# Kernel tuning notes

Hardware: AMD Instinct MI355X
Metric: run time of the kernel (lower is better)

The kernel has to match this reference:

```python
import jax, jax.numpy as jnp
import numpy as np

B, N, E_PER = 512, 256, 8192          # graphs, nodes per graph, edges per graph
FIN, H, K, FOUT = 128, 32, 16, 10     # in_channels, hidden, num clusters, out_channels
EPS = 1e-15


def setup_inputs() -> dict:
    key = jax.random.key(0)
    ks = jax.random.split(key, 12)
    x = jax.random.normal(ks[0], (B * N, FIN), jnp.float32)
    # intra-graph random edges, then offset into the global node index space
    src = jax.random.randint(ks[1], (B, E_PER), 0, N)
    dst = jax.random.randint(ks[2], (B, E_PER), 0, N)
    offs = (jnp.arange(B) * N)[:, None]
    edge_index = jnp.stack([(src + offs).reshape(-1), (dst + offs).reshape(-1)]).astype(jnp.int64)
    batch = jnp.repeat(jnp.arange(B), N).astype(jnp.int64)

    def lin(k, fin, fout):
        return (jax.random.normal(k, (fin, fout), jnp.float32) / np.sqrt(fin)).astype(jnp.float32)

    params = {
        'W_lin1': lin(ks[3], FIN, H), 'b_lin1': jnp.zeros((H,), jnp.float32),
        'W_rel1': lin(ks[4], H, H), 'b_rel1': jnp.zeros((H,), jnp.float32),
        'W_root1': lin(ks[5], H, H),
        'W_pool': lin(ks[6], H, K), 'b_pool': jnp.zeros((K,), jnp.float32),
        'W_rel2': lin(ks[7], H, H), 'b_rel2': jnp.zeros((H,), jnp.float32),
        'W_root2': lin(ks[8], H, H),
        'W_lin2': lin(ks[9], H, H), 'b_lin2': jnp.zeros((H,), jnp.float32),
        'W_lin3': lin(ks[10], H, FOUT), 'b_lin3': jnp.zeros((FOUT,), jnp.float32),
    }
    return {'x': x, 'edge_index': edge_index, 'batch': batch, **params}


def _densify(x, edge_index, batch):
    """to_dense_adj + to_dense_batch: [total,F] -> [B,N,F], [B,N,N], [B,N]."""
    n_total = x.shape[0]
    counts = jax.ops.segment_sum(jnp.ones((n_total,), jnp.int32), batch, num_segments=B)
    offsets = jnp.concatenate([jnp.zeros((1,), jnp.int32), jnp.cumsum(counts)[:-1]])
    pos = jnp.arange(n_total) - offsets[batch]            # position of node inside its graph
    eb = batch[edge_index[0]]                             # graph id of each edge
    adj = jnp.zeros((B, N, N), jnp.float32).at[eb, pos[edge_index[0]], pos[edge_index[1]]].add(1.0)
    xd = jnp.zeros((B, N, x.shape[1]), jnp.float32).at[batch, pos].set(x)
    mask = jnp.zeros((B, N), jnp.float32).at[batch, pos].set(1.0)
    return xd, adj, mask


def _dense_graph_conv(x, adj, W_rel, b_rel, W_root):
    # PyG DenseGraphConv(aggr='add'): lin_rel(adj @ x) + lin_root(x)
    return jnp.einsum('bnm,bmh,hk->bnk', adj, x, W_rel) + b_rel + x @ W_root


def _dense_mincut_pool(x, adj, s, mask):
    s = jax.nn.softmax(s, axis=-1)
    x = x * mask[..., None]
    s = s * mask[..., None]
    out = jnp.einsum('bnk,bnh->bkh', s, x)                        # s^T x
    out_adj = jnp.einsum('bnk,bnm,bmj->bkj', s, adj, s)           # s^T A s
    mincut_num = jnp.einsum('bkk->b', out_adj)
    d_flat = adj.sum(-1)                                          # degree
    mincut_den = jnp.einsum('bnk,bn,bnk->b', s, d_flat, s)        # trace(s^T D s)
    mincut_loss = jnp.mean(-(mincut_num / mincut_den))
    ss = jnp.einsum('bnk,bnj->bkj', s, s)
    ss_norm = jnp.linalg.norm(ss, axis=(-1, -2), keepdims=True)
    i_s = jnp.eye(K, dtype=jnp.float32)
    ortho_loss = jnp.mean(jnp.linalg.norm(ss / ss_norm - i_s / jnp.sqrt(jnp.float32(K)), axis=(-1, -2)))
    # zero diagonal, symmetric degree normalization
    diag_mask = 1.0 - i_s
    out_adj = out_adj * diag_mask
    d = jnp.sqrt(out_adj.sum(-1))[:, None, :] + EPS               # [B,1,K]
    out_adj = out_adj / d / jnp.swapaxes(d, 1, 2)
    return out, out_adj, mincut_loss, ortho_loss


def reference(x, edge_index, batch, W_lin1, b_lin1, W_rel1, b_rel1, W_root1,
              W_pool, b_pool, W_rel2, b_rel2, W_root2, W_lin2, b_lin2, W_lin3, b_lin3):
    xd, adj, mask = _densify(x, edge_index, batch)
    h = xd @ W_lin1 + b_lin1                                      # lin1
    h = _dense_graph_conv(h, adj, W_rel1, b_rel1, W_root1)        # conv1
    s2 = h @ W_pool + b_pool                                      # pool2
    h, adj_p, mincut_loss2, ortho_loss2 = _dense_mincut_pool(h, adj, s2, mask)
    h = _dense_graph_conv(h, adj_p, W_rel2, b_rel2, W_root2)      # conv2
    h = h.sum(axis=1)                                             # readout sum over clusters
    h = jax.nn.relu(h @ W_lin2 + b_lin2)
    h = h @ W_lin3 + b_lin3
    return jax.nn.log_softmax(h, axis=-1), mincut_loss2, ortho_loss2
```

## Files before the change

kernel.cpp:

```cpp
#include <hip/hip_runtime.h>

#define NB 512
#define NN 256
#define EPG 8192
#define FINC 128

typedef float f32x4 __attribute__((ext_vector_type(4)));
typedef short s16x8 __attribute__((ext_vector_type(8)));

__device__ __forceinline__ float bf2f(unsigned short u) {
  union { unsigned int i; float f; } x; x.i = ((unsigned int)u) << 16; return x.f;
}
__device__ __forceinline__ unsigned short f2bf(float f) {
  union { float f; unsigned int i; } x; x.f = f;
  unsigned int r = x.i + 0x7fffu + ((x.i >> 16) & 1u);
  return (unsigned short)(r >> 16);
}
__device__ __forceinline__ short ftrunc_bf(float f) {
  union { float f; unsigned int i; } x; x.f = f;
  return (short)(x.i >> 16);
}

struct Params {
  const void* x; const void* ei;
  const void *wl1, *bl1, *wr1, *br1, *wro1, *wp, *bp;
  const void *wr2, *br2, *wro2, *wl2, *bl2, *wl3, *bl3;
  float* out; float* ws;
};

__device__ __forceinline__ bool detect_bf16(const void* p) {
  const unsigned short* pw = (const unsigned short*)p;
  int sane = 0;
  for (int i = 0; i < 64; ++i) {
    unsigned e = (pw[i] >> 7) & 0xFFu;
    sane += (e > 96u && e < 132u) ? 1 : 0;
  }
  return sane >= 56;
}
__device__ __forceinline__ bool detect_i64(const void* p) {
  const int* pi = (const int*)p + EPG;
  int ok = 0;
  for (int i = 0; i < 32; ++i) ok += (pi[i] >= 256 && pi[i] < 512) ? 1 : 0;
  return ok < 24;
}
__device__ __forceinline__ float ldf(const void* p, int i, bool bf) {
  return bf ? bf2f(((const unsigned short*)p)[i]) : ((const float*)p)[i];
}

#define SMEM_TOTAL 81920

__global__ __launch_bounds__(1024, 8) void mincut_main(Params P) {
  extern __shared__ char smem[];
  const int t = threadIdx.x;
  const int b = blockIdx.x;

  const bool BF  = detect_bf16(P.wr1);
  const bool I64 = detect_i64(P.ei);

  float* pbuf   = (float*)(smem + 0);
  float* oadjb  = (float*)(smem + 2048);
  float* ssb    = (float*)(smem + 3072);
  float* qbuf   = (float*)(smem + 4096);
  float* ddb    = (float*)(smem + 6144);
  float* h2b    = (float*)(smem + 6208);
  float* rb     = (float*)(smem + 8256);
  float* yb     = (float*)(smem + 8384);
  float* lgb    = (float*)(smem + 8512);
  float* scr    = (float*)(smem + 8704);
  float* rel2f  = (float*)(smem + 9216);
  float* root2f = (float*)(smem + 13312);
  float* lin2f  = (float*)(smem + 17408);
  float* lin3f  = (float*)(smem + 21504);
  float* brel2f = (float*)(smem + 22784);
  float* blin2f = (float*)(smem + 22912);
  float* blin3f = (float*)(smem + 23040);
  float* pbufH  = (float*)(smem + 24576);
  float* pbufL  = (float*)(smem + 26624);
  float* oadjH  = (float*)(smem + 28672);
  float* oadjL  = (float*)(smem + 29696);
  float* ssA    = (float*)(smem + 30720);
  float* ssX    = (float*)(smem + 31744);
  unsigned short* h0T  = (unsigned short*)(smem + 33792);
  unsigned short* yTl  = (unsigned short*)(smem + 33792);
  unsigned short* h1Th = (unsigned short*)(smem + 33792);
  unsigned short* w1t  = (unsigned short*)(smem + 50688);
  unsigned short* zT   = (unsigned short*)(smem + 50688);
  unsigned short* sTh  = (unsigned short*)(smem + 50688);
  unsigned short* sTl  = (unsigned short*)(smem + 59136);
  unsigned short* wrelTh = (unsigned short*)(smem + 67584);
  unsigned short* wrelTl = (unsigned short*)(smem + 70144);
  unsigned short* wrootT = (unsigned short*)(smem + 72704);
  float* blin1f = (float*)(smem + 75264);
  unsigned short* yTh = (unsigned short*)(smem + 67584);
  unsigned short* taT = (unsigned short*)(smem + 67584);
  unsigned short* wpoolTh = (unsigned short*)(smem + 76032);
  unsigned short* wpoolTl = (unsigned short*)(smem + 77184);
  unsigned short* m1Th    = (unsigned short*)(smem + 78336);
  unsigned short* m1Tl    = (unsigned short*)(smem + 79488);
  float*          scrE    = (float*)(smem + 79488);
  unsigned short* m2Th    = (unsigned short*)(smem + 80640);
  float*          bMf     = (float*)(smem + 81792);
  unsigned short* brel1h  = (unsigned short*)(smem + 81856);

  const int wv = t >> 6, lane = t & 63;
  const int lm = lane & 15, quad = lane >> 4;
  const int mbase = wv * 16;

  {
    uint4 z = {0u, 0u, 0u, 0u};
    for (int i = t; i < 2112; i += 1024) ((uint4*)smem)[i] = z;
  }
  for (int e = t; e < 4096; e += 1024) {
    int k = e >> 5, c = e & 31;
    w1t[c * 136 + k] = f2bf(ldf(P.wl1, e, BF));
  }
  {
    int k = t >> 5, c = t & 31;
    float wr = ldf(P.wr1, t, BF);
    unsigned short hi = f2bf(wr);
    wrelTh[c * 40 + k] = hi;
    wrelTl[c * 40 + k] = f2bf(wr - bf2f(hi));
    wrootT[c * 40 + k] = f2bf(ldf(P.wro1, t, BF));
  }
  if (t < 512) {
    int m = t >> 4, c = t & 15;
    float w = ldf(P.wp, t, BF);
    unsigned short hi = f2bf(w);
    wpoolTh[c * 36 + m] = hi;
    wpoolTl[c * 36 + m] = f2bf(w - bf2f(hi));
  }
  if (t < 32) { blin1f[t] = ldf(P.bl1, t, BF); brel1h[t] = f2bf(ldf(P.br1, t, BF)); }
  __syncthreads();

  if (I64) {
    const uint4* s4 = (const uint4*)((const long long*)P.ei + (size_t)b * EPG) + t * 4;
    const uint4* d4 = (const uint4*)((const long long*)P.ei + (size_t)NB * EPG + (size_t)b * EPG) + t * 4;
    #pragma unroll
    for (int i = 0; i < 4; ++i) {
      uint4 a = s4[i], c = d4[i];
      unsigned n0 = (a.x & 255u) * 264u + (c.x & 255u);
      unsigned n1 = (a.z & 255u) * 264u + (c.z & 255u);
      atomicAdd((unsigned int*)(smem + ((n0 >> 3) << 2)), 1u << ((n0 & 7u) * 4u));
      atomicAdd((unsigned int*)(smem + ((n1 >> 3) << 2)), 1u << ((n1 & 7u) * 4u));
    }
  } else {
    const uint4* s4 = (const uint4*)((const int*)P.ei + (size_t)b * EPG) + t * 2;
    const uint4* d4 = (const uint4*)((const int*)P.ei + (size_t)NB * EPG + (size_t)b * EPG) + t * 2;
    #pragma unroll
    for (int i = 0; i < 2; ++i) {
      uint4 a = s4[i], c = d4[i];
      unsigned n0 = (a.x & 255u) * 264u + (c.x & 255u);
      unsigned n1 = (a.y & 255u) * 264u + (c.y & 255u);
      unsigned n2 = (a.z & 255u) * 264u + (c.z & 255u);
      unsigned n3 = (a.w & 255u) * 264u + (c.w & 255u);
      atomicAdd((unsigned int*)(smem + ((n0 >> 3) << 2)), 1u << ((n0 & 7u) * 4u));
      atomicAdd((unsigned int*)(smem + ((n1 >> 3) << 2)), 1u << ((n1 & 7u) * 4u));
      atomicAdd((unsigned int*)(smem + ((n2 >> 3) << 2)), 1u << ((n2 & 7u) * 4u));
      atomicAdd((unsigned int*)(smem + ((n3 >> 3) << 2)), 1u << ((n3 & 7u) * 4u));
    }
  }

  {
    f32x4 acc[2] = {{0.f,0.f,0.f,0.f},{0.f,0.f,0.f,0.f}};
    const size_t node = (size_t)(b * 256 + mbase + lm);
    #pragma unroll
    for (int ks = 0; ks < 4; ++ks) {
      const int k0 = ks * 32 + quad * 8;
      s16x8 a;
      if (BF) {
        a = *(const s16x8*)((const unsigned short*)P.x + node * 128 + k0);
      } else {
        const float* xp = (const float*)P.x + node * 128 + k0;
        f32x4 v0 = *(const f32x4*)xp;
        f32x4 v1 = *(const f32x4*)(xp + 4);
        #pragma unroll
        for (int j = 0; j < 4; ++j) { a[j] = (short)f2bf(v0[j]); a[4 + j] = (short)f2bf(v1[j]); }
      }
      #pragma unroll
      for (int ct = 0; ct < 2; ++ct) {
        s16x8 bh = *(const s16x8*)(w1t + (ct * 16 + lm) * 136 + k0);
        acc[ct] = __builtin_amdgcn_mfma_f32_16x16x32_bf16(a, bh, acc[ct], 0, 0, 0);
      }
    }
    #pragma unroll
    for (int ct = 0; ct < 2; ++ct) {
      const int c = ct * 16 + lm;
      float bias = blin1f[c];
      #pragma unroll
      for (int r = 0; r < 4; ++r)
        h0T[c * 264 + mbase + quad * 4 + r] = f2bf(acc[ct][r] + bias);
    }
  }

  if (wv == 2 || wv == 3) {
    const int mb = (wv - 2) * 16;
    s16x8 Ah, Al;
    #pragma unroll
    for (int j = 0; j < 8; ++j) {
      int k = quad * 8 + j;
      Ah[j] = (short)wrelTh[k * 40 + mb + lm];
      Al[j] = (short)wrelTl[k * 40 + mb + lm];
    }
    s16x8 Bh, Bl;
    ((uint2*)&Bh)[0] = *(const uint2*)(wpoolTh + lm * 36 + quad * 8);
    ((uint2*)&Bh)[1] = *(const uint2*)(wpoolTh + lm * 36 + quad * 8 + 4);
    ((uint2*)&Bl)[0] = *(const uint2*)(wpoolTl + lm * 36 + quad * 8);
    ((uint2*)&Bl)[1] = *(const uint2*)(wpoolTl + lm * 36 + quad * 8 + 4);
    f32x4 acc = {0.f, 0.f, 0.f, 0.f};
    acc = __builtin_amdgcn_mfma_f32_16x16x32_bf16(Ah, Bh, acc, 0, 0, 0);
    acc = __builtin_amdgcn_mfma_f32_16x16x32_bf16(Al, Bh, acc, 0, 0, 0);
    acc = __builtin_amdgcn_mfma_f32_16x16x32_bf16(Ah, Bl, acc, 0, 0, 0);
    #pragma unroll
    for (int r = 0; r < 4; ++r) {
      int m = mb + quad * 4 + r;
      unsigned short hi = f2bf(acc[r]);
      m1Th[lm * 36 + m] = hi;
      m1Tl[lm * 36 + m] = f2bf(acc[r] - bf2f(hi));
    }
  }
  if (wv == 4 || wv == 5) {
    const int mb = (wv - 4) * 16;
    s16x8 Ah;
    #pragma unroll
    for (int j = 0; j < 8; ++j) Ah[j] = (short)wrootT[(quad * 8 + j) * 40 + mb + lm];
    s16x8 Bh, Bl;
    ((uint2*)&Bh)[0] = *(const uint2*)(wpoolTh + lm * 36 + quad * 8);
    ((uint2*)&Bh)[1] = *(const uint2*)(wpoolTh + lm * 36 + quad * 8 + 4);
    ((uint2*)&Bl)[0] = *(const uint2*)(wpoolTl + lm * 36 + quad * 8);
    ((uint2*)&Bl)[1] = *(const uint2*)(wpoolTl + lm * 36 + quad * 8 + 4);
    f32x4 acc = {0.f, 0.f, 0.f, 0.f};
    acc = __builtin_amdgcn_mfma_f32_16x16x32_bf16(Ah, Bh, acc, 0, 0, 0);
    acc = __builtin_amdgcn_mfma_f32_16x16x32_bf16(Ah, Bl, acc, 0, 0, 0);
    #pragma unroll
    for (int r = 0; r < 4; ++r) m2Th[lm * 36 + (mb + quad * 4 + r)] = f2bf(acc[r]);
  }
  if (wv == 6 && lane < 16) {
    float acc = ldf(P.bp, lane, BF);
    #pragma unroll 8
    for (int m = 0; m < 32; ++m)
      acc += bf2f(brel1h[m]) * (bf2f(wpoolTh[lane * 36 + m]) + bf2f(wpoolTl[lane * 36 + m]));
    bMf[lane] = acc;
  }
  __syncthreads();

  f32x4 racc[2] = {{0.f,0.f,0.f,0.f},{0.f,0.f,0.f,0.f}};
  f32x4 yacc = {0.f,0.f,0.f,0.f}, macc = {0.f,0.f,0.f,0.f};
  {
    s16x8 Ah;
    #pragma unroll
    for (int j = 0; j < 8; ++j) Ah[j] = (short)h0T[(quad * 8 + j) * 264 + mbase + lm];
    f32x4 zacc[2] = {{0.f,0.f,0.f,0.f},{0.f,0.f,0.f,0.f}};
    #pragma unroll
    for (int ct = 0; ct < 2; ++ct) {
      const int c = ct * 16 + lm;
      s16x8 brh = *(const s16x8*)(wrelTh + c * 40 + quad * 8);
      s16x8 brl = *(const s16x8*)(wrelTl + c * 40 + quad * 8);
      s16x8 bro = *(const s16x8*)(wrootT + c * 40 + quad * 8);
      zacc[ct] = __builtin_amdgcn_mfma_f32_16x16x32_bf16(Ah, brh, zacc[ct], 0, 0, 0);
      zacc[ct] = __builtin_amdgcn_mfma_f32_16x16x32_bf16(Ah, brl, zacc[ct], 0, 0, 0);
      racc[ct] = __builtin_amdgcn_mfma_f32_16x16x32_bf16(Ah, bro, racc[ct], 0, 0, 0);
    }
    s16x8 Bm1h, Bm1l, Bm2;
    ((uint2*)&Bm1h)[0] = *(const uint2*)(m1Th + lm * 36 + quad * 8);
    ((uint2*)&Bm1h)[1] = *(const uint2*)(m1Th + lm * 36 + quad * 8 + 4);
    ((uint2*)&Bm1l)[0] = *(const uint2*)(m1Tl + lm * 36 + quad * 8);
    ((uint2*)&Bm1l)[1] = *(const uint2*)(m1Tl + lm * 36 + quad * 8 + 4);
    ((uint2*)&Bm2)[0]  = *(const uint2*)(m2Th + lm * 36 + quad * 8);
    ((uint2*)&Bm2)[1]  = *(const uint2*)(m2Th + lm * 36 + quad * 8 + 4);
    yacc = __builtin_amdgcn_mfma_f32_16x16x32_bf16(Ah, Bm1h, yacc, 0, 0, 0);
    yacc = __builtin_amdgcn_mfma_f32_16x16x32_bf16(Ah, Bm1l, yacc, 0, 0, 0);
    macc = __builtin_amdgcn_mfma_f32_16x16x32_bf16(Ah, Bm2, macc, 0, 0, 0);
    #pragma unroll
    for (int ct = 0; ct < 2; ++ct)
      #pragma unroll
      for (int r = 0; r < 4; ++r)
        zT[(ct * 16 + lm) * 264 + mbase + quad * 4 + r] = f2bf(zacc[ct][r]);
  }
  __syncthreads();

  #pragma unroll
  for (int r = 0; r < 4; ++r) {
    int node = mbase + quad * 4 + r;
    unsigned short hi = f2bf(yacc[r]);
    yTh[lm * 264 + node] = hi;
    yTl[lm * 264 + node] = f2bf(yacc[r] - bf2f(hi));
  }
  __syncthreads();

  f32x4 h1v[2], sval;
  {
    f32x4 h1acc[2] = { racc[0], racc[1] };
    f32x4 lacc = macc;
    unsigned dsum = 0;
    const char* arow = smem + (mbase + lm) * 132;
    #pragma unroll
    for (int ks = 0; ks < 8; ++ks) {
      unsigned d = *(const unsigned int*)(arow + ks * 16 + quad * 4);
      unsigned v = (d & 0x0F0F0F0Fu) + ((d >> 4) & 0x0F0F0F0Fu);
      dsum += (v * 0x01010101u) >> 24;
      s16x8 af;
      #pragma unroll
      for (int j = 0; j < 8; ++j) af[j] = ftrunc_bf((float)((d >> (4 * j)) & 15u));
      const int v0 = ks * 32 + quad * 8;
      #pragma unroll
      for (int ct = 0; ct < 2; ++ct) {
        s16x8 bz = *(const s16x8*)(zT + (ct * 16 + lm) * 264 + v0);
        h1acc[ct] = __builtin_amdgcn_mfma_f32_16x16x32_bf16(af, bz, h1acc[ct], 0, 0, 0);
      }
      s16x8 byh = *(const s16x8*)(yTh + lm * 264 + v0);
      s16x8 byl = *(const s16x8*)(yTl + lm * 264 + v0);
      lacc = __builtin_amdgcn_mfma_f32_16x16x32_bf16(af, byh, lacc, 0, 0, 0);
      lacc = __builtin_amdgcn_mfma_f32_16x16x32_bf16(af, byl, lacc, 0, 0, 0);
    }
    dsum += __shfl_xor(dsum, 16, 64);
    dsum += __shfl_xor(dsum, 32, 64);
    float degf = (float)dsum;
    #pragma unroll
    for (int ct = 0; ct < 2; ++ct) {
      float bias = bf2f(brel1h[ct * 16 + lm]);
      #pragma unroll
      for (int r = 0; r < 4; ++r) h1v[ct][r] = h1acc[ct][r] + bias;
    }
    f32x4 lg;
    float bm = bMf[lm];
    #pragma unroll
    for (int r = 0; r < 4; ++r) lg[r] = lacc[r] + bm;
    f32x4 mx = lg;
    #pragma unroll
    for (int m = 1; m <= 8; m <<= 1)
      #pragma unroll
      for (int r = 0; r < 4; ++r) mx[r] = fmaxf(mx[r], __shfl_xor(mx[r], m, 64));
    #pragma unroll
    for (int r = 0; r < 4; ++r) lg[r] = __expf(lg[r] - mx[r]);
    f32x4 sm = lg;
    #pragma unroll
    for (int m = 1; m <= 8; m <<= 1)
      #pragma unroll
      for (int r = 0; r < 4; ++r) sm[r] += __shfl_xor(sm[r], m, 64);
    f32x4 sq;
    #pragma unroll
    for (int r = 0; r < 4; ++r) { sval[r] = lg[r] / sm[r]; sq[r] = sval[r] * sval[r]; }
    #pragma unroll
    for (int m = 1; m <= 8; m <<= 1)
      #pragma unroll
      for (int r = 0; r < 4; ++r) sq[r] += __shfl_xor(sq[r], m, 64);
    {
      int l = lane & 15, src = (l >> 2) << 4;
      float q0 = __shfl(sq[0], src, 64), q1 = __shfl(sq[1], src, 64);
      float q2 = __shfl(sq[2], src, 64), q3 = __shfl(sq[3], src, 64);
      float ssel = (l & 2) ? ((l & 1) ? q3 : q2) : ((l & 1) ? q1 : q0);
      float vden = (lane < 16) ? degf * ssel : 0.f;
      #pragma unroll
      for (int o = 32; o > 0; o >>= 1) vden += __shfl_xor(vden, o, 64);
      if (lane == 0) scrE[wv] = vden;
    }
  }
  __syncthreads();

  #pragma unroll
  for (int ct = 0; ct < 2; ++ct)
    #pragma unroll
    for (int r = 0; r < 4; ++r)
      h1Th[(ct * 16 + lm) * 264 + mbase + quad * 4 + r] = f2bf(h1v[ct][r]);
  #pragma unroll
  for (int r = 0; r < 4; ++r) {
    int node = mbase + quad * 4 + r;
    unsigned short hi = f2bf(sval[r]);
    sTh[lm * 264 + node] = hi;
    sTl[lm * 264 + node] = f2bf(sval[r] - bf2f(hi));
  }
  __syncthreads();

  {
    f32x4 tacc = {0.f, 0.f, 0.f, 0.f};
    const char* arow = smem + (mbase + lm) * 132;
    #pragma unroll
    for (int ks = 0; ks < 8; ++ks) {
      unsigned d = *(const unsigned int*)(arow + ks * 16 + quad * 4);
      s16x8 af;
      #pragma unroll
      for (int j = 0; j < 8; ++j) af[j] = ftrunc_bf((float)((d >> (4 * j)) & 15u));
      const int v0 = ks * 32 + quad * 8;
      s16x8 bh = *(const s16x8*)(sTh + lm * 264 + v0);
      s16x8 bl = *(const s16x8*)(sTl + lm * 264 + v0);
      tacc = __builtin_amdgcn_mfma_f32_16x16x32_bf16(af, bh, tacc, 0, 0, 0);
      tacc = __builtin_amdgcn_mfma_f32_16x16x32_bf16(af, bl, tacc, 0, 0, 0);
    }
    #pragma unroll
    for (int r = 0; r < 4; ++r) taT[lm * 264 + mbase + quad * 4 + r] = f2bf(tacc[r]);
  }
  __syncthreads();

  rel2f[t] = ldf(P.wr2, t, BF);
  root2f[t] = ldf(P.wro2, t, BF);
  lin2f[t] = ldf(P.wl2, t, BF);
  if (t < 320) lin3f[t] = ldf(P.wl3, t, BF);
  if (t < 32) brel2f[t] = ldf(P.br2, t, BF);
  if (t < 32) blin2f[t] = ldf(P.bl2, t, BF);
  if (t < 10) blin3f[t] = ldf(P.bl3, t, BF);

  if (wv < 8) {
    const unsigned short *Ap, *Bp; float* dst; int W, ct = 0;
    switch (wv) {
      case 0: Ap = sTh; Bp = h1Th; dst = pbufH; W = 32; ct = 0; break;
      case 1: Ap = sTh; Bp = h1Th; dst = pbufH; W = 32; ct = 1; break;
      case 2: Ap = sTl; Bp = h1Th; dst = pbufL; W = 32; ct = 0; break;
      case 3: Ap = sTl; Bp = h1Th; dst = pbufL; W = 32; ct = 1; break;
      case 4: Ap = sTh; Bp = taT;  dst = oadjH; W = 16; break;
      case 5: Ap = sTl; Bp = taT;  dst = oadjL; W = 16; break;
      case 6: Ap = sTh; Bp = sTh;  dst = ssA;   W = 16; break;
      default: Ap = sTh; Bp = sTl; dst = ssX;   W = 16; break;
    }
    const int cidx = ct * 16 + lm;
    const unsigned short* Bb = Bp + cidx * 264;
    f32x4 acc = {0.f, 0.f, 0.f, 0.f};
    #pragma unroll
    for (int ch = 0; ch < 8; ++ch) {
      s16x8 a = *(const s16x8*)(Ap + lm * 264 + ch * 32 + quad * 8);
      s16x8 bb = *(const s16x8*)(Bb + ch * 32 + quad * 8);
      acc = __builtin_amdgcn_mfma_f32_16x16x32_bf16(a, bb, acc, 0, 0, 0);
    }
    #pragma unroll
    for (int r = 0; r < 4; ++r) dst[(quad * 4 + r) * W + cidx] = acc[r];
  }
  __syncthreads();

  if (t < 512) {
    pbuf[t] = pbufH[t] + pbufL[t];
  } else if (t < 768) {
    int i = t - 512; oadjb[i] = oadjH[i] + oadjL[i];
  } else {
    int i = t - 768; int k3 = i >> 4, j3 = i & 15;
    ssb[i] = ssA[i] + ssX[i] + ssX[j3 * 16 + k3];
  }
  __syncthreads();

  {
    float vnum = (t < 16) ? oadjb[t * 17] : 0.f;
    float vfro = (t < 256) ? ssb[t] * ssb[t] : 0.f;
    float vtr  = (t < 16) ? ssb[t * 17] : 0.f;
    #pragma unroll
    for (int o = 32; o > 0; o >>= 1) {
      vnum += __shfl_xor(vnum, o, 64);
      vfro += __shfl_xor(vfro, o, 64);
      vtr  += __shfl_xor(vtr, o, 64);
    }
    if (lane == 0) { scr[16 + wv] = vnum; scr[32 + wv] = vfro; scr[48 + wv] = vtr; }
  }
  __syncthreads();

  if (t == 0) {
    float den = 0.f, num = 0.f, fro = 0.f, tr = 0.f;
    #pragma unroll
    for (int i = 0; i < 16; ++i) { den += scrE[i]; num += scr[16 + i]; fro += scr[32 + i]; tr += scr[48 + i]; }
    float ssn = sqrtf(fro);
    float orth2 = 2.f - tr / (2.f * ssn);
    atomicAdd(P.ws, -(num / den) * (1.f / NB));
    atomicAdd(P.ws + 1, sqrtf(fmaxf(orth2, 0.f)) * (1.f / NB));
  }
  if (t < 16) {
    float rs = 0.f;
    #pragma unroll
    for (int j = 0; j < 16; ++j) if (j != t) rs += oadjb[t * 16 + j];
    ddb[t] = sqrtf(rs) + 1e-15f;
  }
  __syncthreads();
  if (t < 256) {
    int k = t >> 4, j = t & 15;
    float apv = (k == j) ? 0.f : oadjb[t] / (ddb[k] * ddb[j]);
    oadjb[t] = apv;
  }
  __syncthreads();

  if (t < 512) {
    int k = t >> 5, c = t & 31;
    float q = 0.f;
    #pragma unroll
    for (int j = 0; j < 16; ++j) q += oadjb[k * 16 + j] * pbuf[j * 32 + c];
    qbuf[k * 32 + c] = q;
  }
  __syncthreads();
  if (t < 512) {
    int k = t >> 5, c = t & 31;
    float s0 = 0.f;
    #pragma unroll
    for (int m = 0; m < 32; ++m)
      s0 += qbuf[k * 32 + m] * rel2f[m * 32 + c] + pbuf[k * 32 + m] * root2f[m * 32 + c];
    h2b[k * 32 + c] = s0;
  }
  __syncthreads();

  if (wv == 0) {
    if (lane < 32) {
      float r = 16.f * brel2f[lane];
      #pragma unroll
      for (int k = 0; k < 16; ++k) r += h2b[k * 32 + lane];
      rb[lane] = r;
    }
    if (lane < 32) {
      float y = blin2f[lane];
      #pragma unroll
      for (int m = 0; m < 32; ++m) y += rb[m] * lin2f[m * 32 + lane];
      yb[lane] = fmaxf(y, 0.f);
    }
    if (lane < 10) {
      float lg = blin3f[lane];
      #pragma unroll
      for (int m = 0; m < 32; ++m) lg += yb[m] * lin3f[m * 10 + lane];
      lgb[lane] = lg;
    }
    if (lane == 0) {
      float mx = lgb[0];
      #pragma unroll
      for (int i = 1; i < 10; ++i) mx = fmaxf(mx, lgb[i]);
      float sum = 0.f;
      #pragma unroll
      for (int i = 0; i < 10; ++i) sum += __expf(lgb[i] - mx);
      lgb[10] = mx + __logf(sum);
    }
    if (lane < 10) {
      float val = lgb[lane] - lgb[10];
      if (BF) ((unsigned short*)P.out)[b * 10 + lane] = f2bf(val);
      else    P.out[b * 10 + lane] = val;
    }
  }
}

__global__ void mincut_fin(Params P) {
  if (threadIdx.x == 0) {
    const bool BF = detect_bf16(P.wr1);
    if (BF) {
      ((unsigned short*)P.out)[5120] = f2bf(P.ws[0]);
      ((unsigned short*)P.out)[5121] = f2bf(P.ws[1]);
    } else {
      P.out[5120] = P.ws[0];
      P.out[5121] = P.ws[1];
    }
  }
}

extern "C" void kernel_launch(void* const* d_in, const int* in_sizes, int n_in,
                              void* d_out, int out_size, void* d_ws, size_t ws_size,
                              hipStream_t stream) {
  (void)in_sizes; (void)n_in; (void)out_size; (void)ws_size;
  Params P;
  P.x    = d_in[0];
  P.ei   = d_in[1];
  P.wl1  = d_in[3];
  P.bl1  = d_in[4];
  P.wr1  = d_in[5];
  P.br1  = d_in[6];
  P.wro1 = d_in[7];
  P.wp   = d_in[8];
  P.bp   = d_in[9];
  P.wr2  = d_in[10];
  P.br2  = d_in[11];
  P.wro2 = d_in[12];
  P.wl2  = d_in[13];
  P.bl2  = d_in[14];
  P.wl3  = d_in[15];
  P.bl3  = d_in[16];
  P.out  = (float*)d_out;
  P.ws   = (float*)d_ws;

  hipMemsetAsync(d_ws, 0, 2 * sizeof(float), stream);
  hipFuncSetAttribute(reinterpret_cast<const void*>(mincut_main),
                      hipFuncAttributeMaxDynamicSharedMemorySize, SMEM_TOTAL);
  hipLaunchKernelGGL(mincut_main, dim3(NB), dim3(1024), SMEM_TOTAL, stream, P);
  hipLaunchKernelGGL(mincut_fin, dim3(1), dim3(64), 0, stream, P);
}
```

Measured before the change: 169.9 us.

## Compute pool logits from materialized h1 and decode adjacency nibbles via bit tricks

Drops the precomputed W_rel·W_pool and W_root·W_pool products and the y=A·(z·Wpool) MFMA path. h1 is now written to LDS first and the pool logits are computed directly from h1 with a small MFMA, which adds one barrier but removes several MFMAs and LDS buffers. Adjacency nibbles are decoded to bf16 with an OR-bias trick (16+d encoded as 0x4180|d<<3), and the resulting constant offset is removed using column sums accumulated with LDS atomics. Stores are packed into uint2 writes. The bias-correction scheme adds atomics and slightly changes rounding behaviour.

```diff
diff --git a/kernel.cpp b/kernel.cpp
--- a/kernel.cpp
+++ b/kernel.cpp
@@ -16,9 +16,18 @@
   unsigned int r = x.i + 0x7fffu + ((x.i >> 16) & 1u);
   return (unsigned short)(r >> 16);
 }
-__device__ __forceinline__ short ftrunc_bf(float f) {
-  union { float f; unsigned int i; } x; x.f = f;
-  return (short)(x.i >> 16);
+__device__ __forceinline__ unsigned pk2(unsigned short a, unsigned short c) {
+  return (unsigned)a | ((unsigned)c << 16);
+}
+
+union U16x8 { uint4 u; s16x8 s; };
+__device__ __forceinline__ s16x8 dec8(unsigned d) {
+  U16x8 o;
+  o.u.x = 0x41804180u | ((d & 0x0000000Fu) << 3)  | ((d & 0x000000F0u) << 15);
+  o.u.y = 0x41804180u | ((d & 0x00000F00u) >> 5)  | ((d & 0x0000F000u) << 7);
+  o.u.z = 0x41804180u | ((d & 0x000F0000u) >> 13) | ((d & 0x00F00000u) >> 1);
+  o.u.w = 0x41804180u | ((d & 0x0F000000u) >> 21) | ((d & 0xF0000000u) >> 9);
+  return o.s;
 }
 
 struct Params {
@@ -81,7 +90,6 @@
   float* ssA    = (float*)(smem + 30720);
   float* ssX    = (float*)(smem + 31744);
   unsigned short* h0T  = (unsigned short*)(smem + 33792);
-  unsigned short* yTl  = (unsigned short*)(smem + 33792);
   unsigned short* h1Th = (unsigned short*)(smem + 33792);
   unsigned short* w1t  = (unsigned short*)(smem + 50688);
   unsigned short* zT   = (unsigned short*)(smem + 50688);
@@ -91,15 +99,13 @@
   unsigned short* wrelTl = (unsigned short*)(smem + 70144);
   unsigned short* wrootT = (unsigned short*)(smem + 72704);
   float* blin1f = (float*)(smem + 75264);
-  unsigned short* yTh = (unsigned short*)(smem + 67584);
   unsigned short* taT = (unsigned short*)(smem + 67584);
   unsigned short* wpoolTh = (unsigned short*)(smem + 76032);
   unsigned short* wpoolTl = (unsigned short*)(smem + 77184);
-  unsigned short* m1Th    = (unsigned short*)(smem + 78336);
-  unsigned short* m1Tl    = (unsigned short*)(smem + 79488);
-  float*          scrE    = (float*)(smem + 79488);
-  unsigned short* m2Th    = (unsigned short*)(smem + 80640);
-  float*          bMf     = (float*)(smem + 81792);
+  float*          colzF   = (float*)(smem + 78336);
+  float*          colsF   = (float*)(smem + 78464);
+  float*          scrE    = (float*)(smem + 78528);
+  float*          bpf     = (float*)(smem + 78592);
   unsigned short* brel1h  = (unsigned short*)(smem + 81856);
 
   const int wv = t >> 6, lane = t & 63;
@@ -110,6 +116,7 @@
     uint4 z = {0u, 0u, 0u, 0u};
     for (int i = t; i < 2112; i += 1024) ((uint4*)smem)[i] = z;
   }
+  if (t < 48) colzF[t] = 0.f;
   for (int e = t; e < 4096; e += 1024) {
     int k = e >> 5, c = e & 31;
     w1t[c * 136 + k] = f2bf(ldf(P.wl1, e, BF));
@@ -130,6 +137,7 @@
     wpoolTl[c * 36 + m] = f2bf(w - bf2f(hi));
   }
   if (t < 32) { blin1f[t] = ldf(P.bl1, t, BF); brel1h[t] = f2bf(ldf(P.br1, t, BF)); }
+  if (t < 16) bpf[t] = ldf(P.bp, t, BF);
   __syncthreads();
 
   if (I64) {
@@ -186,65 +194,14 @@
     for (int ct = 0; ct < 2; ++ct) {
       const int c = ct * 16 + lm;
       float bias = blin1f[c];
-      #pragma unroll
-      for (int r = 0; r < 4; ++r)
-        h0T[c * 264 + mbase + quad * 4 + r] = f2bf(acc[ct][r] + bias);
-    }
-  }
-
-  if (wv == 2 || wv == 3) {
-    const int mb = (wv - 2) * 16;
-    s16x8 Ah, Al;
-    #pragma unroll
-    for (int j = 0; j < 8; ++j) {
-      int k = quad * 8 + j;
-      Ah[j] = (short)wrelTh[k * 40 + mb + lm];
-      Al[j] = (short)wrelTl[k * 40 + mb + lm];
-    }
-    s16x8 Bh, Bl;
-    ((uint2*)&Bh)[0] = *(const uint2*)(wpoolTh + lm * 36 + quad * 8);
-    ((uint2*)&Bh)[1] = *(const uint2*)(wpoolTh + lm * 36 + quad * 8 + 4);
-    ((uint2*)&Bl)[0] = *(const uint2*)(wpoolTl + lm * 36 + quad * 8);
-    ((uint2*)&Bl)[1] = *(const uint2*)(wpoolTl + lm * 36 + quad * 8 + 4);
-    f32x4 acc = {0.f, 0.f, 0.f, 0.f};
-    acc = __builtin_amdgcn_mfma_f32_16x16x32_bf16(Ah, Bh, acc, 0, 0, 0);
-    acc = __builtin_amdgcn_mfma_f32_16x16x32_bf16(Al, Bh, acc, 0, 0, 0);
-    acc = __builtin_amdgcn_mfma_f32_16x16x32_bf16(Ah, Bl, acc, 0, 0, 0);
-    #pragma unroll
-    for (int r = 0; r < 4; ++r) {
-      int m = mb + quad * 4 + r;
-      unsigned short hi = f2bf(acc[r]);
-      m1Th[lm * 36 + m] = hi;
-      m1Tl[lm * 36 + m] = f2bf(acc[r] - bf2f(hi));
-    }
-  }
-  if (wv == 4 || wv == 5) {
-    const int mb = (wv - 4) * 16;
-    s16x8 Ah;
-    #pragma unroll
-    for (int j = 0; j < 8; ++j) Ah[j] = (short)wrootT[(quad * 8 + j) * 40 + mb + lm];
-    s16x8 Bh, Bl;
-    ((uint2*)&Bh)[0] = *(const uint2*)(wpoolTh + lm * 36 + quad * 8);
-    ((uint2*)&Bh)[1] = *(const uint2*)(wpoolTh + lm * 36 + quad * 8 + 4);
-    ((uint2*)&Bl)[0] = *(const uint2*)(wpoolTl + lm * 36 + quad * 8);
-    ((uint2*)&Bl)[1] = *(const uint2*)(wpoolTl + lm * 36 + quad * 8 + 4);
-    f32x4 acc = {0.f, 0.f, 0.f, 0.f};
-    acc = __builtin_amdgcn_mfma_f32_16x16x32_bf16(Ah, Bh, acc, 0, 0, 0);
-    acc = __builtin_amdgcn_mfma_f32_16x16x32_bf16(Ah, Bl, acc, 0, 0, 0);
-    #pragma unroll
-    for (int r = 0; r < 4; ++r) m2Th[lm * 36 + (mb + quad * 4 + r)] = f2bf(acc[r]);
-  }
-  if (wv == 6 && lane < 16) {
-    float acc = ldf(P.bp, lane, BF);
-    #pragma unroll 8
-    for (int m = 0; m < 32; ++m)
-      acc += bf2f(brel1h[m]) * (bf2f(wpoolTh[lane * 36 + m]) + bf2f(wpoolTl[lane * 36 + m]));
-    bMf[lane] = acc;
+      *(uint2*)(h0T + c * 264 + mbase + quad * 4) =
+          make_uint2(pk2(f2bf(acc[ct][0] + bias), f2bf(acc[ct][1] + bias)),
+                     pk2(f2bf(acc[ct][2] + bias), f2bf(acc[ct][3] + bias)));
+    }
   }
   __syncthreads();
 
   f32x4 racc[2] = {{0.f,0.f,0.f,0.f},{0.f,0.f,0.f,0.f}};
-  f32x4 yacc = {0.f,0.f,0.f,0.f}, macc = {0.f,0.f,0.f,0.f};
   {
     s16x8 Ah;
     #pragma unroll
@@ -260,37 +217,23 @@
       zacc[ct] = __builtin_amdgcn_mfma_f32_16x16x32_bf16(Ah, brl, zacc[ct], 0, 0, 0);
       racc[ct] = __builtin_amdgcn_mfma_f32_16x16x32_bf16(Ah, bro, racc[ct], 0, 0, 0);
     }
-    s16x8 Bm1h, Bm1l, Bm2;
-    ((uint2*)&Bm1h)[0] = *(const uint2*)(m1Th + lm * 36 + quad * 8);
-    ((uint2*)&Bm1h)[1] = *(const uint2*)(m1Th + lm * 36 + quad * 8 + 4);
-    ((uint2*)&Bm1l)[0] = *(const uint2*)(m1Tl + lm * 36 + quad * 8);
-    ((uint2*)&Bm1l)[1] = *(const uint2*)(m1Tl + lm * 36 + quad * 8 + 4);
-    ((uint2*)&Bm2)[0]  = *(const uint2*)(m2Th + lm * 36 + quad * 8);
-    ((uint2*)&Bm2)[1]  = *(const uint2*)(m2Th + lm * 36 + quad * 8 + 4);
-    yacc = __builtin_amdgcn_mfma_f32_16x16x32_bf16(Ah, Bm1h, yacc, 0, 0, 0);
-    yacc = __builtin_amdgcn_mfma_f32_16x16x32_bf16(Ah, Bm1l, yacc, 0, 0, 0);
-    macc = __builtin_amdgcn_mfma_f32_16x16x32_bf16(Ah, Bm2, macc, 0, 0, 0);
-    #pragma unroll
-    for (int ct = 0; ct < 2; ++ct)
-      #pragma unroll
-      for (int r = 0; r < 4; ++r)
-        zT[(ct * 16 + lm) * 264 + mbase + quad * 4 + r] = f2bf(zacc[ct][r]);
-  }
-  __syncthreads();
-
-  #pragma unroll
-  for (int r = 0; r < 4; ++r) {
-    int node = mbase + quad * 4 + r;
-    unsigned short hi = f2bf(yacc[r]);
-    yTh[lm * 264 + node] = hi;
-    yTl[lm * 264 + node] = f2bf(yacc[r] - bf2f(hi));
-  }
-  __syncthreads();
-
-  f32x4 h1v[2], sval;
+    #pragma unroll
+    for (int ct = 0; ct < 2; ++ct) {
+      unsigned short u0 = f2bf(zacc[ct][0]), u1 = f2bf(zacc[ct][1]);
+      unsigned short u2 = f2bf(zacc[ct][2]), u3 = f2bf(zacc[ct][3]);
+      *(uint2*)(zT + (ct * 16 + lm) * 264 + mbase + quad * 4) =
+          make_uint2(pk2(u0, u1), pk2(u2, u3));
+      float pz = (bf2f(u0) + bf2f(u1)) + (bf2f(u2) + bf2f(u3));
+      pz += __shfl_xor(pz, 16, 64);
+      pz += __shfl_xor(pz, 32, 64);
+      if (lane < 16) atomicAdd(colzF + ct * 16 + lm, pz);
+    }
+  }
+  __syncthreads();
+
+  float degf;
   {
     f32x4 h1acc[2] = { racc[0], racc[1] };
-    f32x4 lacc = macc;
     unsigned dsum = 0;
     const char* arow = smem + (mbase + lm) * 132;
     #pragma unroll
@@ -298,31 +241,42 @@
       unsigned d = *(const unsigned int*)(arow + ks * 16 + quad * 4);
       unsigned v = (d & 0x0F0F0F0Fu) + ((d >> 4) & 0x0F0F0F0Fu);
       dsum += (v * 0x01010101u) >> 24;
-      s16x8 af;
-      #pragma unroll
-      for (int j = 0; j < 8; ++j) af[j] = ftrunc_bf((float)((d >> (4 * j)) & 15u));
+      s16x8 af = dec8(d);
       const int v0 = ks * 32 + quad * 8;
       #pragma unroll
       for (int ct = 0; ct < 2; ++ct) {
         s16x8 bz = *(const s16x8*)(zT + (ct * 16 + lm) * 264 + v0);
         h1acc[ct] = __builtin_amdgcn_mfma_f32_16x16x32_bf16(af, bz, h1acc[ct], 0, 0, 0);
       }
-      s16x8 byh = *(const s16x8*)(yTh + lm * 264 + v0);
-      s16x8 byl = *(const s16x8*)(yTl + lm * 264 + v0);
-      lacc = __builtin_amdgcn_mfma_f32_16x16x32_bf16(af, byh, lacc, 0, 0, 0);
-      lacc = __builtin_amdgcn_mfma_f32_16x16x32_bf16(af, byl, lacc, 0, 0, 0);
     }
     dsum += __shfl_xor(dsum, 16, 64);
     dsum += __shfl_xor(dsum, 32, 64);
-    float degf = (float)dsum;
+    degf = (float)dsum;
     #pragma unroll
     for (int ct = 0; ct < 2; ++ct) {
-      float bias = bf2f(brel1h[ct * 16 + lm]);
-      #pragma unroll
-      for (int r = 0; r < 4; ++r) h1v[ct][r] = h1acc[ct][r] + bias;
-    }
+      const int c = ct * 16 + lm;
+      float bias = bf2f(brel1h[c]) - 16.f * colzF[c];
+      *(uint2*)(h1Th + c * 264 + mbase + quad * 4) =
+          make_uint2(pk2(f2bf(h1acc[ct][0] + bias), f2bf(h1acc[ct][1] + bias)),
+                     pk2(f2bf(h1acc[ct][2] + bias), f2bf(h1acc[ct][3] + bias)));
+    }
+  }
+  __syncthreads();
+
+  {
+    s16x8 Ah1;
+    #pragma unroll
+    for (int j = 0; j < 8; ++j) Ah1[j] = (short)h1Th[(quad * 8 + j) * 264 + mbase + lm];
+    s16x8 Bh, Bl;
+    ((uint2*)&Bh)[0] = *(const uint2*)(wpoolTh + lm * 36 + quad * 8);
+    ((uint2*)&Bh)[1] = *(const uint2*)(wpoolTh + lm * 36 + quad * 8 + 4);
+    ((uint2*)&Bl)[0] = *(const uint2*)(wpoolTl + lm * 36 + quad * 8);
+    ((uint2*)&Bl)[1] = *(const uint2*)(wpoolTl + lm * 36 + quad * 8 + 4);
+    f32x4 lacc = {0.f, 0.f, 0.f, 0.f};
+    lacc = __builtin_amdgcn_mfma_f32_16x16x32_bf16(Ah1, Bh, lacc, 0, 0, 0);
+    lacc = __builtin_amdgcn_mfma_f32_16x16x32_bf16(Ah1, Bl, lacc, 0, 0, 0);
     f32x4 lg;
-    float bm = bMf[lm];
+    float bm = bpf[lm];
     #pragma unroll
     for (int r = 0; r < 4; ++r) lg[r] = lacc[r] + bm;
     f32x4 mx = lg;
@@ -337,13 +291,26 @@
     for (int m = 1; m <= 8; m <<= 1)
       #pragma unroll
       for (int r = 0; r < 4; ++r) sm[r] += __shfl_xor(sm[r], m, 64);
-    f32x4 sq;
+    f32x4 sval, sq;
     #pragma unroll
     for (int r = 0; r < 4; ++r) { sval[r] = lg[r] / sm[r]; sq[r] = sval[r] * sval[r]; }
     #pragma unroll
     for (int m = 1; m <= 8; m <<= 1)
       #pragma unroll
       for (int r = 0; r < 4; ++r) sq[r] += __shfl_xor(sq[r], m, 64);
+    {
+      unsigned short h0s = f2bf(sval[0]); float r0 = bf2f(h0s); unsigned short l0 = f2bf(sval[0] - r0);
+      unsigned short h1s = f2bf(sval[1]); float r1 = bf2f(h1s); unsigned short l1 = f2bf(sval[1] - r1);
+      unsigned short h2s = f2bf(sval[2]); float r2 = bf2f(h2s); unsigned short l2 = f2bf(sval[2] - r2);
+      unsigned short h3s = f2bf(sval[3]); float r3 = bf2f(h3s); unsigned short l3 = f2bf(sval[3] - r3);
+      const int nb = lm * 264 + mbase + quad * 4;
+      *(uint2*)(sTh + nb) = make_uint2(pk2(h0s, h1s), pk2(h2s, h3s));
+      *(uint2*)(sTl + nb) = make_uint2(pk2(l0, l1), pk2(l2, l3));
+      float sr = ((r0 + bf2f(l0)) + (r1 + bf2f(l1))) + ((r2 + bf2f(l2)) + (r3 + bf2f(l3)));
+      sr += __shfl_xor(sr, 16, 64);
+      sr += __shfl_xor(sr, 32, 64);
+      if (lane < 16) atomicAdd(colsF + lm, sr);
+    }
     {
       int l = lane & 15, src = (l >> 2) << 4;
       float q0 = __shfl(sq[0], src, 64), q1 = __shfl(sq[1], src, 64);
@@ -357,37 +324,24 @@
   }
   __syncthreads();
 
-  #pragma unroll
-  for (int ct = 0; ct < 2; ++ct)
-    #pragma unroll
-    for (int r = 0; r < 4; ++r)
-      h1Th[(ct * 16 + lm) * 264 + mbase + quad * 4 + r] = f2bf(h1v[ct][r]);
-  #pragma unroll
-  for (int r = 0; r < 4; ++r) {
-    int node = mbase + quad * 4 + r;
-    unsigned short hi = f2bf(sval[r]);
-    sTh[lm * 264 + node] = hi;
-    sTl[lm * 264 + node] = f2bf(sval[r] - bf2f(hi));
-  }
-  __syncthreads();
-
-  {
+  {
+    float cols = colsF[lm];
     f32x4 tacc = {0.f, 0.f, 0.f, 0.f};
     const char* arow = smem + (mbase + lm) * 132;
     #pragma unroll
     for (int ks = 0; ks < 8; ++ks) {
       unsigned d = *(const unsigned int*)(arow + ks * 16 + quad * 4);
-      s16x8 af;
-      #pragma unroll
-      for (int j = 0; j < 8; ++j) af[j] = ftrunc_bf((float)((d >> (4 * j)) & 15u));
+      s16x8 af = dec8(d);
       const int v0 = ks * 32 + quad * 8;
       s16x8 bh = *(const s16x8*)(sTh + lm * 264 + v0);
       s16x8 bl = *(const s16x8*)(sTl + lm * 264 + v0);
       tacc = __builtin_amdgcn_mfma_f32_16x16x32_bf16(af, bh, tacc, 0, 0, 0);
       tacc = __builtin_amdgcn_mfma_f32_16x16x32_bf16(af, bl, tacc, 0, 0, 0);
     }
-    #pragma unroll
-    for (int r = 0; r < 4; ++r) taT[lm * 264 + mbase + quad * 4 + r] = f2bf(tacc[r]);
+    float c16 = 16.f * cols;
+    *(uint2*)(taT + lm * 264 + mbase + quad * 4) =
+        make_uint2(pk2(f2bf(tacc[0] - c16), f2bf(tacc[1] - c16)),
+                   pk2(f2bf(tacc[2] - c16), f2bf(tacc[3] - c16)));
   }
   __syncthreads();
 
```

Measured after the change: 170.1 us. No clear change (+0.1%).
